# Kernel optimization log

Measured on AMD Instinct MI355X. Metric: run time of the kernel, lower is better.

Reference implementation:

```python
import jax, jax.numpy as jnp
import numpy as np

NH, NKV, HD, ROPE_DIMS, ROPE_BASE = 16, 4, 128, 64, 10000.0


def _rms_norm(x):
    eps = jnp.asarray(jnp.finfo(x.dtype).eps, x.dtype)
    return x * jax.lax.rsqrt(jnp.mean(x * x, axis=-1, keepdims=True) + eps)


def _apply_rope_partial(x, cos, sin):
    # x: [B, H, T, hd]; cos/sin: [T, rope_dims//2]
    h = ROPE_DIMS // 2
    xa, xb, xp = x[..., :h], x[..., h:ROPE_DIMS], x[..., ROPE_DIMS:]
    c, s = cos[None, None], sin[None, None]
    rot = jnp.concatenate([xa * c - xb * s, xa * s + xb * c], axis=-1)
    return jnp.concatenate([rot, xp], axis=-1)


def setup_inputs() -> dict:
    key = jax.random.key(0)
    ks = jax.random.split(key, 7)
    B, T, D = 2, 2048, 2048
    kv_dim = NKV * HD
    sc = lambda n: 1.0 / np.sqrt(n)
    return {
        "x": jax.random.normal(ks[0], (B, T, D), jnp.float32),
        "ve_embed": jax.random.normal(ks[1], (B, T, kv_dim), jnp.float32),
        "Wq": jax.random.normal(ks[2], (D, D), jnp.float32) * sc(D),
        "Wk": jax.random.normal(ks[3], (kv_dim, D), jnp.float32) * sc(D),
        "Wv": jax.random.normal(ks[4], (kv_dim, D), jnp.float32) * sc(D),
        "Wproj": jax.random.normal(ks[5], (D, D), jnp.float32) * sc(D),
        "q_gain": jnp.full((NH,), 12.0, jnp.float32)
        + 0.01 * jax.random.normal(ks[6], (NH,), jnp.float32),
    }


def reference(x, ve_embed, Wq, Wk, Wv, Wproj, q_gain):
    B, T, D = x.shape
    g = NH // NKV  # GQA group size

    # QKV projections -> [B, H, T, hd]
    q = (x @ Wq.T).reshape(B, T, NH, HD).transpose(0, 2, 1, 3)
    k = (x @ Wk.T).reshape(B, T, NKV, HD).transpose(0, 2, 1, 3)
    v = (x @ Wv.T).reshape(B, T, NKV, HD).transpose(0, 2, 1, 3)

    q, k = _rms_norm(q), _rms_norm(k)

    # partial RoPE (frequencies built over full hd, first rope_dims//2 used)
    inv_freq = 1.0 / ROPE_BASE ** (jnp.arange(0, HD, 2, dtype=jnp.float32) / HD)
    f = jnp.arange(T, dtype=jnp.float32)[:, None] * inv_freq[None, :]  # [T, hd//2]
    cos, sin = jnp.cos(f)[:, : ROPE_DIMS // 2], jnp.sin(f)[:, : ROPE_DIMS // 2]
    q = _apply_rope_partial(q, cos, sin)
    k = _apply_rope_partial(k, cos, sin)

    q = q * q_gain[None, :, None, None]
    v = v + ve_embed.reshape(B, T, NKV, HD).transpose(0, 2, 1, 3)

    # GQA causal attention: q grouped as [B, nkv, g, T, hd]
    qg = q.reshape(B, NKV, g, T, HD)
    scale = 1.0 / np.sqrt(HD)
    scores = jnp.einsum("bkgtd,bksd->bkgts", qg, k) * scale
    causal = jnp.tril(jnp.ones((T, T), bool))
    scores = jnp.where(causal[None, None, None], scores, -jnp.inf)
    p = jax.nn.softmax(scores, axis=-1)
    y = jnp.einsum("bkgts,bksd->bkgtd", p, v)  # [B, nkv, g, T, hd]

    y = y.reshape(B, NH, T, HD).transpose(0, 2, 1, 3).reshape(B, T, D)
    return y @ Wproj.T
```

## Files before the change

### kernel.cpp

```cpp
#include <hip/hip_runtime.h>
#include <hip/hip_bf16.h>
#include <cstdint>
#include <cstddef>


typedef _Float16 f16_t;
typedef f16_t f16x4 __attribute__((ext_vector_type(4)));
typedef f16_t f16x8 __attribute__((ext_vector_type(8)));
typedef float f32x4 __attribute__((ext_vector_type(4)));

#define MFMA16F(a, b, c) __builtin_amdgcn_mfma_f32_16x16x32_f16((a), (b), (c), 0, 0, 0)
#define SBAR()   __builtin_amdgcn_s_barrier()
#define SCHED0() __builtin_amdgcn_sched_barrier(0)
#define LGKM0()  asm volatile("s_waitcnt lgkmcnt(0)" ::: "memory")

__device__ __forceinline__ void gload16(const f16_t* g, f16_t* l) {
  auto lds_ptr = reinterpret_cast<__attribute__((address_space(3))) unsigned int*>(
      reinterpret_cast<uintptr_t>(l));
  auto g_ptr = reinterpret_cast<const __attribute__((address_space(1))) unsigned int*>(
      reinterpret_cast<uintptr_t>(g));
  __builtin_amdgcn_global_load_lds(g_ptr, lds_ptr, 16, 0, 0);
}

__device__ __forceinline__ void cast4(const float* __restrict__ s, f16_t* __restrict__ d) {
  const float4 v = *reinterpret_cast<const float4*>(s);
  f16_t r[4] = {(f16_t)v.x, (f16_t)v.y, (f16_t)v.z, (f16_t)v.w};
  *reinterpret_cast<uint64_t*>(d) = *reinterpret_cast<const uint64_t*>(r);
}

__global__ __launch_bounds__(256) void k_prep(
    const float* __restrict__ x, const float* __restrict__ Wq,
    const float* __restrict__ Wk, const float* __restrict__ Wv,
    const float* __restrict__ Wp, f16_t* __restrict__ xf,
    f16_t* __restrict__ wqkvf, f16_t* __restrict__ wpf,
    float* __restrict__ ctab, float* __restrict__ stab)
{
  const long N4X = 2097152;
  const long N4W = 1572864;
  const long N4P = 1048576;
  const long N4R = 16384;
  long i = (long)blockIdx.x * blockDim.x + threadIdx.x;
  const long step = (long)gridDim.x * blockDim.x;
  for (; i < N4X + N4W + N4P + N4R; i += step) {
    if (i < N4X) {
      cast4(x + i * 4, xf + i * 4);
    } else if (i < N4X + N4W) {
      const long j = (i - N4X) * 4;
      const long row = j >> 11, col = j & 2047;
      const float* src = (row < 2048) ? (Wq + row * 2048)
                       : (row < 2560) ? (Wk + (row - 2048) * 2048)
                                      : (Wv + (row - 2560) * 2048);
      cast4(src + col, wqkvf + j);
    } else if (i < N4X + N4W + N4P) {
      const long j = (i - N4X - N4W) * 4;
      cast4(Wp + j, wpf + j);
    } else {
      const long j = (i - N4X - N4W - N4P) * 4;
#pragma unroll
      for (int k = 0; k < 4; ++k) {
        const long idx = j + k;
        const int t = (int)(idx >> 5), fi = (int)(idx & 31);
        const float freq = exp2f(-(float)fi * 0.2076205059304601f);
        const float f = (float)t * freq;
        ctab[idx] = cosf(f);
        stab[idx] = sinf(f);
      }
    }
  }
}

__global__ __launch_bounds__(256) void k_vtrans(
    const f16_t* __restrict__ vn, f16_t* __restrict__ vt)
{
  __shared__ __align__(16) f16_t lsT[64 * 136];
  const int t0 = blockIdx.x * 64;
  const int bk = blockIdx.y;
  const f16_t* src = vn + ((size_t)bk * 2048 + t0) * 128;
  f16_t* dst = vt + (size_t)bk * 128 * 2048;
  const int tid = threadIdx.x;
#pragma unroll
  for (int it = 0; it < 4; ++it) {
    const int cch = tid + it * 256;
    const int r = cch >> 4, c = cch & 15;
    *reinterpret_cast<f16x8*>(&lsT[r * 136 + c * 8]) =
        *reinterpret_cast<const f16x8*>(src + (size_t)r * 128 + c * 8);
  }
  __syncthreads();
#pragma unroll
  for (int it = 0; it < 4; ++it) {
    const int u = tid + it * 256;
    const int d = u >> 3, c8 = u & 7;
    f16_t vals[8];
#pragma unroll
    for (int j = 0; j < 8; ++j) vals[j] = lsT[(c8 * 8 + j) * 136 + d];
    *reinterpret_cast<f16x8*>(dst + (size_t)d * 2048 + t0 + c8 * 8) =
        *reinterpret_cast<const f16x8*>(vals);
  }
}

template <int NBU, typename OutT>
__global__ __launch_bounds__(1024, 1) void k_gemmQ(
    const f16_t* __restrict__ A, const f16_t* __restrict__ Bm,
    OutT* __restrict__ C, int M, int N, int K, int lda, int ldb)
{
  __shared__ __align__(16) f16_t lds[2][(4 + NBU) * 4096];
  const int tid = threadIdx.x;
  const int l = tid & 63, w = tid >> 6;
  const int lrow = l & 15, lk = l >> 4;
  const int wm = w >> 2, wn = w & 3;

  const int nwg = gridDim.x * gridDim.y;
  int lin = blockIdx.y * gridDim.x + blockIdx.x;
  lin = (lin & 7) * (nwg >> 3) + (lin >> 3);
  const int m0 = (lin / gridDim.x) * 256, n0 = (lin % gridDim.x) * (64 * NBU);

  const bool stager = (tid < 512);
  const int srow = tid >> 3;
  const int scol = ((tid & 7) ^ (srow & 7)) << 3;
  const f16_t* gP[4 + NBU];
#pragma unroll
  for (int u = 0; u < 4; ++u) gP[u] = A + (size_t)(m0 + u * 64 + srow) * lda + scol;
#pragma unroll
  for (int u = 0; u < NBU; ++u) gP[4 + u] = Bm + (size_t)(n0 + u * 64 + srow) * ldb + scol;

  auto stageAll = [&](int buf, int k0) {
#pragma unroll
    for (int u = 0; u < 4 + NBU; ++u)
      gload16(gP[u] + k0, &lds[buf][u * 4096 + tid * 8]);
  };
  auto rdA = [&](int buf, int mf, int ks) -> f16x8 {
    const int row = wm * 64 + mf * 16 + lrow;
    const int slot = ((ks << 2) | lk) ^ (row & 7);
    return *reinterpret_cast<const f16x8*>(&lds[buf][row * 64 + slot * 8]);
  };
  auto rdB = [&](int buf, int nf, int ks) -> f16x8 {
    const int row = wn * (16 * NBU) + nf * 16 + lrow;
    const int slot = ((ks << 2) | lk) ^ (row & 7);
    return *reinterpret_cast<const f16x8*>(&lds[buf][16384 + row * 64 + slot * 8]);
  };

  f32x4 acc[4][NBU] = {};
  const int nkt = K >> 6;

  if (stager) {
    stageAll(0, 0);
    stageAll(1, nkt > 1 ? 64 : 0);
  }
  if constexpr (NBU == 3) { asm volatile("s_waitcnt vmcnt(7)" ::: "memory"); }
  else                    { asm volatile("s_waitcnt vmcnt(6)" ::: "memory"); }
  SCHED0();
  SBAR(); SCHED0();

  f16x8 aA[4][2], bB[NBU][2];
  for (int kt = 0; kt < nkt; ++kt) {
    const int b = kt & 1;
    const int kn2 = (kt + 2 < nkt ? kt + 2 : nkt - 1) << 6;

#pragma unroll
    for (int mf = 0; mf < 4; ++mf) { aA[mf][0] = rdA(b, mf, 0); aA[mf][1] = rdA(b, mf, 1); }
#pragma unroll
    for (int nf = 0; nf < NBU; ++nf) { bB[nf][0] = rdB(b, nf, 0); bB[nf][1] = rdB(b, nf, 1); }
    __builtin_amdgcn_s_setprio(1);
#pragma unroll
    for (int mf = 0; mf < 2; ++mf)
#pragma unroll
      for (int nf = 0; nf < NBU; ++nf)
#pragma unroll
        for (int ks = 0; ks < 2; ++ks)
          acc[mf][nf] = MFMA16F(aA[mf][ks], bB[nf][ks], acc[mf][nf]);
    __builtin_amdgcn_s_setprio(0);
    LGKM0(); SCHED0();
    SBAR(); SCHED0();

    if (stager) stageAll(b, kn2);
    if constexpr (NBU == 3) { asm volatile("s_waitcnt vmcnt(7)" ::: "memory"); }
    else                    { asm volatile("s_waitcnt vmcnt(6)" ::: "memory"); }
    SCHED0();
    __builtin_amdgcn_s_setprio(1);
#pragma unroll
    for (int mf = 2; mf < 4; ++mf)
#pragma unroll
      for (int nf = 0; nf < NBU; ++nf)
#pragma unroll
        for (int ks = 0; ks < 2; ++ks)
          acc[mf][nf] = MFMA16F(aA[mf][ks], bB[nf][ks], acc[mf][nf]);
    __builtin_amdgcn_s_setprio(0);
    SBAR(); SCHED0();
  }

#pragma unroll
  for (int mf = 0; mf < 4; ++mf) {
    const int row = m0 + wm * 64 + mf * 16 + lk * 4;
#pragma unroll
    for (int nf = 0; nf < NBU; ++nf) {
      const int col = n0 + wn * (16 * NBU) + nf * 16 + lrow;
#pragma unroll
      for (int rg = 0; rg < 4; ++rg)
        C[(size_t)(row + rg) * N + col] = (OutT)acc[mf][nf][rg];
    }
  }
  (void)M;
}

__global__ __launch_bounds__(256) void k_qkv_epi(
    const f16_t* __restrict__ qkv, const float* __restrict__ ve,
    const float* __restrict__ qgain,
    const float* __restrict__ ctab, const float* __restrict__ stab,
    f16_t* __restrict__ qn, f16_t* __restrict__ kn, f16_t* __restrict__ vn)
{
  const int blk = blockIdx.x;
  const int b = blk >> 11, t = blk & 2047;
  const int w = threadIdx.x >> 6, l = threadIdx.x & 63;
  const int i32 = l & 31;
  const float c = ctab[t * 32 + i32], s = stab[t * 32 + i32];
  const float EPS = 1.1920929e-07f;
  constexpr float SCALE_L2E = 0.088388347648318447f * 1.4426950408889634f;

#pragma unroll
  for (int it = 0; it < 4; ++it) {
    const int h = w + it * 4;
    const f16_t* row = qkv + (size_t)blk * 3072 + h * 128;
    float x0 = (float)row[l], x1 = (float)row[l + 64];
    float ss = x0 * x0 + x1 * x1;
#pragma unroll
    for (int off = 32; off; off >>= 1) ss += __shfl_xor(ss, off);
    const float rn = rsqrtf(ss * (1.0f / 128.0f) + EPS);
    x0 *= rn; x1 *= rn;
    const float p = __shfl_xor(x0, 32);
    float xr = (l < 32) ? (x0 * c - p * s) : (p * s + x0 * c);
    const float g = qgain[h] * SCALE_L2E;
    xr *= g; x1 *= g;
    f16_t* orow = qn + (((size_t)(b * 16 + h)) * 2048 + t) * 128;
    orow[l] = (f16_t)xr;
    orow[l + 64] = (f16_t)x1;
  }
  {
    const f16_t* row = qkv + (size_t)blk * 3072 + 2048 + w * 128;
    float x0 = (float)row[l], x1 = (float)row[l + 64];
    float ss = x0 * x0 + x1 * x1;
#pragma unroll
    for (int off = 32; off; off >>= 1) ss += __shfl_xor(ss, off);
    const float rn = rsqrtf(ss * (1.0f / 128.0f) + EPS);
    x0 *= rn; x1 *= rn;
    const float p = __shfl_xor(x0, 32);
    const float xr = (l < 32) ? (x0 * c - p * s) : (p * s + x0 * c);
    f16_t* orow = kn + (((size_t)(b * 4 + w)) * 2048 + t) * 128;
    orow[l] = (f16_t)xr;
    orow[l + 64] = (f16_t)x1;
  }
  {
    const f16_t* row = qkv + (size_t)blk * 3072 + 2560 + w * 128;
    const float* verow = ve + (size_t)blk * 512 + w * 128;
    f16_t* orow = vn + (((size_t)(b * 4 + w)) * 2048 + t) * 128;
    orow[l] = (f16_t)((float)row[l] + verow[l]);
    orow[l + 64] = (f16_t)((float)row[l + 64] + verow[l + 64]);
  }
}

__global__ __launch_bounds__(256, 3) void k_attn(
    const f16_t* __restrict__ qn, const f16_t* __restrict__ kn,
    const f16_t* __restrict__ vt, f16_t* __restrict__ y)
{
  __shared__ __align__(16) f16_t lsK[64 * 128];
  __shared__ __align__(16) f16_t lsV[128 * 64];
  __shared__ __align__(16) f16_t lsPb[4][16 * 64];
  const int qt = 31 - (int)blockIdx.y;
  const int bh = blockIdx.x;
  const int b = bh >> 4, h = bh & 15, kvh = h >> 2;
  const int tid = threadIdx.x, w = tid >> 6, l = tid & 63;
  const int lrow = l & 15, lk = l >> 4;
  const int qbase = qt * 64 + w * 16;
  constexpr float NEG = -1e30f;
  f16_t* lsP = lsPb[w];

  const f16_t* qp = qn + ((size_t)(b * 16 + h) * 2048) * 128;
  f16x8 aQ[4];
#pragma unroll
  for (int kf = 0; kf < 4; ++kf)
    aQ[kf] = *reinterpret_cast<const f16x8*>(
        qp + (size_t)(qbase + lrow) * 128 + kf * 32 + lk * 8);

  const f16_t* kp = kn + ((size_t)(b * 4 + kvh) * 2048) * 128;
  const f16_t* vtp = vt + (size_t)(b * 4 + kvh) * 128 * 2048;

  f32x4 o[8] = {};
  float mst = NEG;
  float lst = 0.f;

  f16x8 kreg[4], vreg[4];
  auto loadKV = [&](int t0) {
#pragma unroll
    for (int it = 0; it < 4; ++it) {
      const int cch = tid + it * 256;
      kreg[it] = *reinterpret_cast<const f16x8*>(
          kp + (size_t)(t0 + (cch >> 4)) * 128 + (cch & 15) * 8);
      vreg[it] = *reinterpret_cast<const f16x8*>(
          vtp + (size_t)(cch >> 3) * 2048 + t0 + (cch & 7) * 8);
    }
  };
  loadKV(0);

  const int ntiles = qt + 1;
  for (int tt = 0; tt < ntiles; ++tt) {
    __syncthreads();
#pragma unroll
    for (int it = 0; it < 4; ++it) {
      const int cch = tid + it * 256;
      const int r = cch >> 4, dg = cch & 15;
      *reinterpret_cast<f16x8*>(&lsK[r * 128 + ((dg ^ (r & 7)) << 3)]) = kreg[it];
      const int d = cch >> 3, c8 = cch & 7;
      *reinterpret_cast<f16x8*>(&lsV[d * 64 + ((c8 ^ (d & 7)) << 3)]) = vreg[it];
    }
    if (tt + 1 < ntiles) loadKV((tt + 1) * 64);
    __syncthreads();

    f32x4 sacc[4] = {};
#pragma unroll
    for (int cf = 0; cf < 4; ++cf) {
      const int krow = cf * 16 + lrow;
#pragma unroll
      for (int kf = 0; kf < 4; ++kf) {
        const f16x8 aK = *reinterpret_cast<const f16x8*>(
            &lsK[krow * 128 + ((((kf << 2) | lk) ^ (krow & 7)) << 3)]);
        sacc[cf] = MFMA16F(aK, aQ[kf], sacc[cf]);
      }
    }

    if (tt == qt) {
      const int qin = w * 16 + lrow;
#pragma unroll
      for (int cf = 0; cf < 4; ++cf)
#pragma unroll
        for (int rg = 0; rg < 4; ++rg)
          if (cf * 16 + lk * 4 + rg > qin) sacc[cf][rg] = NEG;
    }

    float mx = NEG;
#pragma unroll
    for (int cf = 0; cf < 4; ++cf)
      mx = fmaxf(mx, fmaxf(fmaxf(sacc[cf][0], sacc[cf][1]),
                           fmaxf(sacc[cf][2], sacc[cf][3])));
    if (__any(mx > mst + 8.f)) {
      float rmx = mx;
      rmx = fmaxf(rmx, __shfl_xor(rmx, 16));
      rmx = fmaxf(rmx, __shfl_xor(rmx, 32));
      const float mnew = fmaxf(mst, rmx);
      const float alpha = exp2f(mst - mnew);
      mst = mnew;
      lst *= alpha;
#pragma unroll
      for (int rg = 0; rg < 4; ++rg) {
        const float arow = __shfl(alpha, lk * 4 + rg);
#pragma unroll
        for (int df = 0; df < 8; ++df) o[df][rg] *= arow;
      }
    }
#pragma unroll
    for (int cf = 0; cf < 4; ++cf) {
#pragma unroll
      for (int rg = 0; rg < 4; ++rg) {
        const float p = exp2f(sacc[cf][rg] - mst);
        sacc[cf][rg] = p;
        lst += p;
      }
    }

#pragma unroll
    for (int cf = 0; cf < 4; ++cf) {
      f16x4 pk;
#pragma unroll
      for (int rg = 0; rg < 4; ++rg) pk[rg] = (f16_t)sacc[cf][rg];
      const int slot8 = cf * 2 + (lk >> 1);
      *reinterpret_cast<f16x4*>(
          &lsP[lrow * 64 + ((slot8 ^ (lrow & 7)) << 3) + (lk & 1) * 4]) = pk;
    }
#pragma unroll
    for (int k2 = 0; k2 < 2; ++k2) {
      const f16x8 aP = *reinterpret_cast<const f16x8*>(
          &lsP[lrow * 64 + ((((k2 << 2) | lk) ^ (lrow & 7)) << 3)]);
#pragma unroll
      for (int df = 0; df < 8; ++df) {
        const int row = df * 16 + lrow;
        const f16x8 bV = *reinterpret_cast<const f16x8*>(
            &lsV[row * 64 + ((((k2 << 2) | lk) ^ (row & 7)) << 3)]);
        o[df] = MFMA16F(aP, bV, o[df]);
      }
    }
  }

  lst += __shfl_xor(lst, 16);
  lst += __shfl_xor(lst, 32);

#pragma unroll
  for (int rg = 0; rg < 4; ++rg) {
    const float lrow_sum = __shfl(lst, lk * 4 + rg);
    const float inv = 1.0f / lrow_sum;
    const int qi = qbase + lk * 4 + rg;
    const size_t rowoff = ((size_t)(b * 2048 + qi)) * 2048 + h * 128;
#pragma unroll
    for (int df = 0; df < 8; ++df)
      y[rowoff + df * 16 + lrow] = (f16_t)(o[df][rg] * inv);
  }
}

extern "C" void kernel_launch(void* const* d_in, const int* in_sizes, int n_in,
                              void* d_out, int out_size, void* d_ws, size_t ws_size,
                              hipStream_t stream) {
  const float* x  = (const float*)d_in[0];
  const float* ve = (const float*)d_in[1];
  const float* Wq = (const float*)d_in[2];
  const float* Wk = (const float*)d_in[3];
  const float* Wv = (const float*)d_in[4];
  const float* Wp = (const float*)d_in[5];
  const float* qg = (const float*)d_in[6];
  float* out = (float*)d_out;

  char* ws = (char*)d_ws;
  size_t off = 0;
  auto alloc = [&](size_t bytes) -> char* {
    char* p = ws + off;
    off += (bytes + 255) & ~(size_t)255;
    return p;
  };

  f16_t* xf    = (f16_t*)alloc((size_t)4096 * 2048 * 2);
  f16_t* wqkvf = (f16_t*)alloc((size_t)3072 * 2048 * 2);
  f16_t* wpf   = (f16_t*)alloc((size_t)2048 * 2048 * 2);
  f16_t* qkvf  = (f16_t*)alloc((size_t)4096 * 3072 * 2);
  f16_t* kn    = (f16_t*)alloc((size_t)2 * 4 * 2048 * 128 * 2);
  f16_t* vn    = (f16_t*)alloc((size_t)2 * 4 * 2048 * 128 * 2);
  f16_t* vt    = (f16_t*)alloc((size_t)2 * 4 * 128 * 2048 * 2);
  float* ctab  = (float*)alloc((size_t)2048 * 32 * 4);
  float* stab  = (float*)alloc((size_t)2048 * 32 * 4);
  f16_t* qn    = xf;
  f16_t* yb    = qkvf;
  (void)ws_size; (void)in_sizes; (void)n_in; (void)out_size;

  k_prep<<<2048, 256, 0, stream>>>(x, Wq, Wk, Wv, Wp, xf, wqkvf, wpf, ctab, stab);

  k_gemmQ<3, f16_t><<<dim3(16, 16), 1024, 0, stream>>>(
      xf, wqkvf, qkvf, 4096, 3072, 2048, 2048, 2048);

  k_qkv_epi<<<4096, 256, 0, stream>>>(qkvf, ve, qg, ctab, stab, qn, kn, vn);

  k_vtrans<<<dim3(32, 8), 256, 0, stream>>>(vn, vt);

  k_attn<<<dim3(32, 32), 256, 0, stream>>>(qn, kn, vt, yb);

  k_gemmQ<2, float><<<dim3(16, 16), 1024, 0, stream>>>(
      yb, wpf, out, 4096, 2048, 2048, 2048, 2048);
}
```

Measured before the change: 188.8 us.

## Split long causal attention rows across two blocks with a combine kernel

The 16 query tiles with the most causal KV tiles (rows 1024 and up) each have their KV range split between two workgroups. Each workgroup writes an unnormalized partial output plus its running max and sum. A new combine kernel merges the two halves with a log-sum-exp rescale. This is meant to shorten the critical path of the longest workgroups and balance load across CUs, at the cost of extra global traffic for the partials and one more kernel launch.

After: 192.0 us. Within noise of the previous version (+1.7%).

```diff
diff --git a/kernel.cpp b/kernel.cpp
--- a/kernel.cpp
+++ b/kernel.cpp
@@ -259,12 +259,23 @@
 
 __global__ __launch_bounds__(256, 3) void k_attn(
     const f16_t* __restrict__ qn, const f16_t* __restrict__ kn,
-    const f16_t* __restrict__ vt, f16_t* __restrict__ y)
+    const f16_t* __restrict__ vt, f16_t* __restrict__ y,
+    f16_t* __restrict__ po, float* __restrict__ pm, float* __restrict__ pl)
 {
   __shared__ __align__(16) f16_t lsK[64 * 128];
   __shared__ __align__(16) f16_t lsV[128 * 64];
   __shared__ __align__(16) f16_t lsPb[4][16 * 64];
-  const int qt = 31 - (int)blockIdx.y;
+  const int j = blockIdx.y;
+  int qt, sp, tstart, tcnt;
+  bool split;
+  if (j < 32) {
+    qt = 31 - (j >> 1); sp = j & 1; split = true;
+    const int tot = qt + 1, c0 = (tot + 1) >> 1;
+    tstart = sp ? c0 : 0;
+    tcnt = sp ? tot - c0 : c0;
+  } else {
+    qt = 47 - j; sp = 0; split = false; tstart = 0; tcnt = qt + 1;
+  }
   const int bh = blockIdx.x;
   const int b = bh >> 4, h = bh & 15, kvh = h >> 2;
   const int tid = threadIdx.x, w = tid >> 6, l = tid & 63;
@@ -298,10 +309,10 @@
           vtp + (size_t)(cch >> 3) * 2048 + t0 + (cch & 7) * 8);
     }
   };
-  loadKV(0);
-
-  const int ntiles = qt + 1;
-  for (int tt = 0; tt < ntiles; ++tt) {
+  loadKV(tstart * 64);
+
+  for (int ti = 0; ti < tcnt; ++ti) {
+    const int tt = tstart + ti;
     __syncthreads();
 #pragma unroll
     for (int it = 0; it < 4; ++it) {
@@ -311,7 +322,7 @@
       const int d = cch >> 3, c8 = cch & 7;
       *reinterpret_cast<f16x8*>(&lsV[d * 64 + ((c8 ^ (d & 7)) << 3)]) = vreg[it];
     }
-    if (tt + 1 < ntiles) loadKV((tt + 1) * 64);
+    if (ti + 1 < tcnt) loadKV((tt + 1) * 64);
     __syncthreads();
 
     f32x4 sacc[4] = {};
@@ -391,15 +402,63 @@
   lst += __shfl_xor(lst, 16);
   lst += __shfl_xor(lst, 32);
 
-#pragma unroll
-  for (int rg = 0; rg < 4; ++rg) {
-    const float lrow_sum = __shfl(lst, lk * 4 + rg);
-    const float inv = 1.0f / lrow_sum;
-    const int qi = qbase + lk * 4 + rg;
-    const size_t rowoff = ((size_t)(b * 2048 + qi)) * 2048 + h * 128;
-#pragma unroll
-    for (int df = 0; df < 8; ++df)
-      y[rowoff + df * 16 + lrow] = (f16_t)(o[df][rg] * inv);
+  if (!split) {
+#pragma unroll
+    for (int rg = 0; rg < 4; ++rg) {
+      const float lrow_sum = __shfl(lst, lk * 4 + rg);
+      const float inv = 1.0f / lrow_sum;
+      const int qi = qbase + lk * 4 + rg;
+      const size_t rowoff = ((size_t)(b * 2048 + qi)) * 2048 + h * 128;
+#pragma unroll
+      for (int df = 0; df < 8; ++df)
+        y[rowoff + df * 16 + lrow] = (f16_t)(o[df][rg] * inv);
+    }
+  } else {
+    const size_t jb = (((size_t)(sp * 2 + b) * 16 + h) * 1024);
+#pragma unroll
+    for (int rg = 0; rg < 4; ++rg) {
+      const int qi = qbase + lk * 4 + rg;
+      f16_t* prow = po + (jb + (qi - 1024)) * 128;
+#pragma unroll
+      for (int df = 0; df < 8; ++df)
+        prow[df * 16 + lrow] = (f16_t)o[df][rg];
+    }
+    if (lk == 0) {
+      const int qi = qbase + lrow;
+      pm[jb + (qi - 1024)] = mst;
+      pl[jb + (qi - 1024)] = lst;
+    }
+  }
+}
+
+__global__ __launch_bounds__(256) void k_combine(
+    const f16_t* __restrict__ po, const float* __restrict__ pm,
+    const float* __restrict__ pl, f16_t* __restrict__ y)
+{
+  const int bh = blockIdx.x;
+  const int b = bh >> 4, h = bh & 15;
+  const int tid = threadIdx.x;
+  const int r = blockIdx.y * 32 + (tid >> 3);
+  const int d0 = (tid & 7) * 16;
+  const size_t base1 = (((size_t)(0 * 2 + b) * 16 + h) * 1024 + r);
+  const size_t base2 = (((size_t)(1 * 2 + b) * 16 + h) * 1024 + r);
+  const float m1 = pm[base1], m2 = pm[base2];
+  const float l1 = pl[base1], l2 = pl[base2];
+  const float m = fmaxf(m1, m2);
+  const float f1 = exp2f(m1 - m), f2 = exp2f(m2 - m);
+  const float inv = 1.0f / (f1 * l1 + f2 * l2);
+  const f16_t* o1 = po + base1 * 128 + d0;
+  const f16_t* o2 = po + base2 * 128 + d0;
+  f16_t* yr = y + ((size_t)(b * 2048 + 1024 + r)) * 2048 + h * 128 + d0;
+#pragma unroll
+  for (int v = 0; v < 2; ++v) {
+    const f16x8 a = *reinterpret_cast<const f16x8*>(o1 + v * 8);
+    const f16x8 c = *reinterpret_cast<const f16x8*>(o2 + v * 8);
+    f16_t outv[8];
+#pragma unroll
+    for (int jj = 0; jj < 8; ++jj)
+      outv[jj] = (f16_t)((f1 * (float)a[jj] + f2 * (float)c[jj]) * inv);
+    *reinterpret_cast<f16x8*>(yr + v * 8) = *reinterpret_cast<const f16x8*>(outv);
   }
 }
 
@@ -430,6 +489,9 @@
   f16_t* kn    = (f16_t*)alloc((size_t)2 * 4 * 2048 * 128 * 2);
   f16_t* vn    = (f16_t*)alloc((size_t)2 * 4 * 2048 * 128 * 2);
   f16_t* vt    = (f16_t*)alloc((size_t)2 * 4 * 128 * 2048 * 2);
+  f16_t* po    = (f16_t*)alloc((size_t)2 * 2 * 16 * 1024 * 128 * 2);
+  float* pm    = (float*)alloc((size_t)2 * 2 * 16 * 1024 * 4);
+  float* pl    = (float*)alloc((size_t)2 * 2 * 16 * 1024 * 4);
   float* ctab  = (float*)alloc((size_t)2048 * 32 * 4);
   float* stab  = (float*)alloc((size_t)2048 * 32 * 4);
   f16_t* qn    = xf;
@@ -445,7 +507,9 @@
 
   k_vtrans<<<dim3(32, 8), 256, 0, stream>>>(vn, vt);
 
-  k_attn<<<dim3(32, 32), 256, 0, stream>>>(qn, kn, vt, yb);
+  k_attn<<<dim3(32, 48), 256, 0, stream>>>(qn, kn, vt, yb, po, pm, pl);
+
+  k_combine<<<dim3(32, 32), 256, 0, stream>>>(po, pm, pl, yb);
 
   k_gemmQ<2, float><<<dim3(16, 16), 1024, 0, stream>>>(
       yb, wpf, out, 4096, 2048, 2048, 2048, 2048);
```
